# Optimization experiments

Hardware: AMD Instinct MI355X
Metric: run time of the kernel (lower is better)

The kernel has to match this reference:

```python
import jax, jax.numpy as jnp
import numpy as np

# Dropout layers are treated as identity (eval mode); note the original Adaptive
# module references self.dropout without defining it, so train mode would error anyway.

def setup_inputs() -> dict:
    key = jax.random.key(0)
    ks = jax.random.split(key, 13)
    B, T, H, E2, VOC, K = 128, 64, 512, 1024, 10000, 49
    s = lambda *sh: 1.0 / np.sqrt(sh[-1])
    return {
        "x":       jax.random.normal(ks[0], (B, T, E2), jnp.float32),
        "hiddens": jax.random.normal(ks[1], (B, T, H), jnp.float32),
        "cells":   jax.random.normal(ks[2], (B, T, H), jnp.float32),
        "V":       jax.random.normal(ks[3], (B, K, H), jnp.float32),
        # attention params
        "Wv": jax.random.normal(ks[4], (K, H), jnp.float32) * s(K, H),
        "Wg": jax.random.normal(ks[5], (K, H), jnp.float32) * s(K, H),
        "Ws": jax.random.normal(ks[6], (K, H), jnp.float32) * s(K, H),
        "wh": jax.random.normal(ks[7], (K,), jnp.float32) * s(K,),
        # sentinel params
        "Wx":  jax.random.normal(ks[8], (H, E2), jnp.float32) * s(H, E2),
        "Wsh": jax.random.normal(ks[9], (H, H), jnp.float32) * s(H, H),
        # output mlp
        "Wm": jax.random.normal(ks[10], (VOC, H), jnp.float32) * s(VOC, H),
        "bm": jnp.zeros((VOC,), jnp.float32),
    }


def reference(x, hiddens, cells, V, Wv, Wg, Ws, wh, Wx, Wsh, Wm, bm):
    B, T, H = hiddens.shape
    # h_{t-1}: zero init state prepended, last hidden dropped
    h0 = jnp.zeros((B, 1, H), hiddens.dtype)
    hiddens_t_1 = jnp.concatenate([h0, hiddens[:, :-1, :]], axis=1) if T > 1 else h0

    # Sentinel gate: sent_t = sigmoid(x Wx^T + h_{t-1} Wh^T) * tanh(cells)
    gate = jnp.einsum('bte,he->bth', x, Wx) + jnp.einsum('btj,hj->bth', hiddens_t_1, Wsh)
    sent = jax.nn.sigmoid(gate) * jnp.tanh(cells)            # [B,T,H]

    # Additive attention over K=49 spatial features
    cv = jnp.einsum('bkh,nh->bkn', V, Wv)                    # [B,K,49]
    cg = jnp.einsum('bth,nh->btn', hiddens, Wg)              # [B,T,49]
    content = jnp.tanh(cv[:, None, :, :] + cg[:, :, None, :])  # [B,T,K,49]
    z = jnp.einsum('btkn,n->btk', content, wh)               # [B,T,K]
    alpha = jax.nn.softmax(z, axis=-1)                       # [B,T,K]
    c = jnp.einsum('btk,bkh->bth', alpha, V)                 # [B,T,H]

    # Sentinel-extended softmax -> beta
    cs = jnp.einsum('bth,nh->btn', sent, Ws) + cg            # [B,T,49]
    z_ext = jnp.einsum('btn,n->bt', jnp.tanh(cs), wh)[..., None]  # [B,T,1]
    extend = jnp.concatenate([z, z_ext], axis=-1)            # [B,T,K+1]
    alpha_hat = jax.nn.softmax(extend, axis=-1)
    beta = alpha_hat[:, :, -1:]                              # [B,T,1]

    c_hat = beta * sent + (1.0 - beta) * c                   # [B,T,H]
    output = jnp.einsum('bth,vh->btv', c_hat + hiddens, Wm) + bm  # [B,T,vocab]
    return output, alpha, beta
```

## Files before the change

### kernel.cpp

```cpp
#include <hip/hip_runtime.h>
#include <hip/hip_bf16.h>
#include <math.h>

typedef __bf16 bf16;
typedef __bf16 bf16x4 __attribute__((ext_vector_type(4)));
typedef __bf16 bf16x8 __attribute__((ext_vector_type(8)));
typedef float f32x4 __attribute__((ext_vector_type(4)));

#define BB  128
#define TT  64
#define BTT 8192
#define HH  512
#define EE  1024
#define KA  49
#define NV  10000

__device__ __forceinline__ float ftanh(float x) {
    float cx = fminf(fmaxf(x, -15.f), 15.f);
    float e = __expf(2.f * cx);
    return (e - 1.f) * __builtin_amdgcn_rcpf(e + 1.f);
}
__device__ __forceinline__ float fsigmoid(float x) {
    return __builtin_amdgcn_rcpf(1.f + __expf(-x));
}

__device__ __forceinline__ void cvt4(const float* __restrict__ s, bf16* __restrict__ d) {
    f32x4 v = *(const f32x4*)s;
    bf16x4 o = { (bf16)v[0], (bf16)v[1], (bf16)v[2], (bf16)v[3] };
    *(bf16x4*)d = o;
}
__device__ __forceinline__ void cvt4nt(const float* __restrict__ s, bf16* __restrict__ d) {
    f32x4 v = __builtin_nontemporal_load((const f32x4*)s);
    bf16x4 o = { (bf16)v[0], (bf16)v[1], (bf16)v[2], (bf16)v[3] };
    *(bf16x4*)d = o;
}

__global__ __launch_bounds__(256)
void prep_kernel(const float* __restrict__ x, const float* __restrict__ hid,
                 const float* __restrict__ V, const float* __restrict__ Wv,
                 const float* __restrict__ Wg, const float* __restrict__ Ws,
                 const float* __restrict__ Wx, const float* __restrict__ Wsh,
                 bf16* __restrict__ xb, bf16* __restrict__ hb, bf16* __restrict__ hpb,
                 bf16* __restrict__ Vb, bf16* __restrict__ Wvb, bf16* __restrict__ Wgb,
                 bf16* __restrict__ Wsb, bf16* __restrict__ Wxb, bf16* __restrict__ Wshb)
{
    const long NX = (long)BTT * EE;
    const long NH = (long)BTT * HH;
    const long NVV = (long)BB * KA * HH;
    const long NWX = (long)HH * EE;
    const long NWSH = (long)HH * HH;
    const long NW = (long)KA * HH;
    const long total4 = (NX + NH + NH + NVV + NWX + NWSH + 3 * NW) >> 2;

    long t0 = (long)blockIdx.x * 256 + threadIdx.x;
    long st = (long)gridDim.x * 256;
    for (long i4 = t0; i4 < total4; i4 += st) {
        long i = i4 << 2;
        if (i < NX) { cvt4nt(x + i, xb + i); continue; }
        i -= NX;
        if (i < NH) { cvt4(hid + i, hb + i); continue; }
        i -= NH;
        if (i < NH) {
            long t = (i >> 9) & (TT - 1);
            if (t == 0) { bf16x4 z = {}; *(bf16x4*)(hpb + i) = z; }
            else cvt4(hid + i - HH, hpb + i);
            continue;
        }
        i -= NH;
        if (i < NVV) { cvt4nt(V + i, Vb + i); continue; }
        i -= NVV;
        if (i < NWX) { cvt4nt(Wx + i, Wxb + i); continue; }
        i -= NWX;
        if (i < NWSH) { cvt4nt(Wsh + i, Wshb + i); continue; }
        i -= NWSH;
        if (i < NW) { cvt4nt(Wv + i, Wvb + i); continue; }
        i -= NW;
        if (i < NW) { cvt4nt(Wg + i, Wgb + i); continue; }
        i -= NW;
        cvt4nt(Ws + i, Wsb + i);
    }
}

template<int EPI>
__device__ __forceinline__ void gemm128_core(
    bf16* smem,
    const bf16* __restrict__ A1, const bf16* __restrict__ B1, int K1,
    const bf16* __restrict__ A2, const bf16* __restrict__ B2, int K2,
    int N, const float* __restrict__ eaux, void* __restrict__ outv, int ldo,
    int bm0, int bn0)
{
    const int tid = threadIdx.x;
    const int lane = tid & 63;
    const int wid = tid >> 6;
    const int wm = (wid >> 1) * 64;
    const int wn = (wid & 1) * 64;
    const int rA = lane & 15;
    const int ks = lane >> 4;
    const int swzB = (ks ^ ((rA >> 1) & 3)) * 16;

    const int c0 = tid, c1 = tid + 256;
    const int row0 = c0 >> 2, row1 = c1 >> 2;
    const int gc0 = ((c0 & 3) ^ ((row0 >> 1) & 3)) * 8;
    const int gc1 = ((c1 & 3) ^ ((row1 >> 1) & 3)) * 8;
    const int br0 = (bn0 + row0 < N) ? bn0 + row0 : N - 1;
    const int br1 = (bn0 + row1 < N) ? bn0 + row1 : N - 1;

    const int NT1 = K1 >> 5;
    const int NT2 = K2 >> 5;
    const int NT = NT1 + NT2;

    auto stage = [&](int t) {
        const bf16 *Ap, *Bp; int K, k0;
        if (t < NT1) { Ap = A1; Bp = B1; K = K1; k0 = t << 5; }
        else         { Ap = A2; Bp = B2; K = K2; k0 = (t - NT1) << 5; }
        char* base = (char*)smem + (t & 3) * 16384;
        __builtin_amdgcn_global_load_lds(
            (const __attribute__((address_space(1))) unsigned int*)(Ap + (size_t)(bm0 + row0) * K + k0 + gc0),
            (__attribute__((address_space(3))) unsigned int*)(base + c0 * 16), 16, 0, 0);
        __builtin_amdgcn_global_load_lds(
            (const __attribute__((address_space(1))) unsigned int*)(Ap + (size_t)(bm0 + row1) * K + k0 + gc1),
            (__attribute__((address_space(3))) unsigned int*)(base + c1 * 16), 16, 0, 0);
        __builtin_amdgcn_global_load_lds(
            (const __attribute__((address_space(1))) unsigned int*)(Bp + (size_t)br0 * K + k0 + gc0),
            (__attribute__((address_space(3))) unsigned int*)(base + 8192 + c0 * 16), 16, 0, 0);
        __builtin_amdgcn_global_load_lds(
            (const __attribute__((address_space(1))) unsigned int*)(Bp + (size_t)br1 * K + k0 + gc1),
            (__attribute__((address_space(3))) unsigned int*)(base + 8192 + c1 * 16), 16, 0, 0);
    };

    f32x4 acc[4][4] = {};

    stage(0); stage(1); stage(2);
    asm volatile("s_waitcnt vmcnt(8)" ::: "memory");
    __builtin_amdgcn_s_barrier();

    for (int t = 0; t < NT; ++t) {
        const char* sA = (const char*)smem + (t & 3) * 16384;
        const char* sB = sA + 8192;

        bf16x8 af[4], bfr[4];
        #pragma unroll
        for (int mi = 0; mi < 4; ++mi)
            af[mi] = *(const bf16x8*)(sA + (wm + mi * 16 + rA) * 64 + swzB);
        #pragma unroll
        for (int ni = 0; ni < 4; ++ni)
            bfr[ni] = *(const bf16x8*)(sB + (wn + ni * 16 + rA) * 64 + swzB);

        if (t + 3 < NT) {
            stage(t + 3);
            asm volatile("s_waitcnt vmcnt(8)" ::: "memory");
        } else if (t + 2 < NT) {
            asm volatile("s_waitcnt vmcnt(4)" ::: "memory");
        } else {
            asm volatile("s_waitcnt vmcnt(0)" ::: "memory");
        }
        __builtin_amdgcn_s_barrier();

        __builtin_amdgcn_s_setprio(1);
        #pragma unroll
        for (int mi = 0; mi < 4; ++mi) {
            #pragma unroll
            for (int ni = 0; ni < 4; ++ni)
                acc[mi][ni] = __builtin_amdgcn_mfma_f32_16x16x32_bf16(af[mi], bfr[ni], acc[mi][ni], 0, 0, 0);
        }
        __builtin_amdgcn_s_setprio(0);
        __builtin_amdgcn_s_barrier();
    }

    #pragma unroll
    for (int mi = 0; mi < 4; ++mi) {
        #pragma unroll
        for (int ni = 0; ni < 4; ++ni) {
            const int col = bn0 + wn + ni * 16 + rA;
            if (col < N) {
                #pragma unroll
                for (int r = 0; r < 4; ++r) {
                    const int rowg = bm0 + wm + mi * 16 + ks * 4 + r;
                    float v = acc[mi][ni][r];
                    if (EPI == 0) {
                        ((bf16*)outv)[(size_t)rowg * ldo + col] =
                            (bf16)(fsigmoid(v) * ftanh(eaux[(size_t)rowg * ldo + col]));
                    } else {
                        ((float*)outv)[(size_t)rowg * ldo + col] = v;
                    }
                }
            }
        }
    }
}

__global__ __launch_bounds__(256, 2)
void gate_mid128(const bf16* __restrict__ xb, const bf16* __restrict__ Wxb,
                 const bf16* __restrict__ hpb, const bf16* __restrict__ Wshb,
                 const float* __restrict__ cel, bf16* __restrict__ sentb,
                 const bf16* __restrict__ Vb, const bf16* __restrict__ Wvb,
                 const bf16* __restrict__ hb, const bf16* __restrict__ Wgb,
                 float* __restrict__ cv, float* __restrict__ cg,
                 const float* __restrict__ Wm, bf16* __restrict__ Wmb)
{
    __shared__ bf16 smem[4 * 8192];
    const int bid = blockIdx.x;
    if (bid >= 369) {
        const long n4 = ((long)NV * HH) >> 2;
        for (long i4 = (long)(bid - 369) * 256 + threadIdx.x; i4 < n4; i4 += 143L * 256)
            cvt4nt(Wm + (i4 << 2), Wmb + (i4 << 2));
        return;
    }
    if (bid < 256) {
        const int bm0 = (bid >> 2) * 128;
        const int bn0 = (bid & 3) * 128;
        gemm128_core<0>(smem, xb, Wxb, EE, hpb, Wshb, HH, HH, cel, (void*)sentb, HH, bm0, bn0);
    } else if (bid < 305) {
        gemm128_core<2>(smem, Vb, Wvb, HH, nullptr, nullptr, 0, KA, nullptr, (void*)cv, KA,
                        (bid - 256) * 128, 0);
    } else {
        gemm128_core<2>(smem, hb, Wgb, HH, nullptr, nullptr, 0, KA, nullptr, (void*)cg, KA,
                        (bid - 305) * 128, 0);
    }
}

__global__ __launch_bounds__(256, 2)
void cs128(const bf16* __restrict__ sentb, const bf16* __restrict__ Wsb,
           const bf16* __restrict__ hb, const bf16* __restrict__ Wgb,
           float* __restrict__ cs)
{
    __shared__ bf16 smem[4 * 8192];
    gemm128_core<2>(smem, sentb, Wsb, HH, hb, Wgb, HH, KA, nullptr, (void*)cs, KA,
                    blockIdx.x * 128, 0);
}

__global__ __launch_bounds__(512, 4)
void gemm256x128_bias(const bf16* __restrict__ A, const bf16* __restrict__ B,
                      const float* __restrict__ bias, float* __restrict__ out)
{
    const int K = HH;
    const int N = NV;
    const int NT = K / 32;
    const int ntn = 79;

    __shared__ bf16 smem[3 * 12288];

    const int bid = blockIdx.x;
    const int wg = (bid & 7) * 316 + (bid >> 3);
    const int bm0 = (wg / ntn) * 256;
    const int bn0 = (wg % ntn) * 128;

    const int tid = threadIdx.x;
    const int lane = tid & 63;
    const int wid = tid >> 6;
    const int wr = (wid >> 1) * 64;
    const int wc = (wid & 1) * 64;
    const int rA = lane & 15;
    const int ks = lane >> 4;
    const int swz = (ks ^ ((rA >> 1) & 3)) * 16;

    const int arow0 = tid >> 2;
    const int arow1 = arow0 + 128;
    const int gcA0 = ((tid & 3) ^ ((arow0 >> 1) & 3)) * 8;
    const int gcA1 = ((tid & 3) ^ ((arow1 >> 1) & 3)) * 8;
    const int brow = tid >> 2;
    const int gcB  = ((tid & 3) ^ ((brow >> 1) & 3)) * 8;
    const int browc = (bn0 + brow < N) ? bn0 + brow : N - 1;

    const bf16* Ap0 = A + (size_t)(bm0 + arow0) * K + gcA0;
    const bf16* Ap1 = A + (size_t)(bm0 + arow1) * K + gcA1;
    const bf16* Bp  = B + (size_t)browc * K + gcB;

    auto stage = [&](int t, int slot) {
        char* base = (char*)smem + slot * 24576;
        const int k0 = t << 5;
        __builtin_amdgcn_global_load_lds(
            (const __attribute__((address_space(1))) unsigned int*)(Ap0 + k0),
            (__attribute__((address_space(3))) unsigned int*)(base + tid * 16), 16, 0, 0);
        __builtin_amdgcn_global_load_lds(
            (const __attribute__((address_space(1))) unsigned int*)(Ap1 + k0),
            (__attribute__((address_space(3))) unsigned int*)(base + (tid + 512) * 16), 16, 0, 0);
        __builtin_amdgcn_global_load_lds(
            (const __attribute__((address_space(1))) unsigned int*)(Bp + k0),
            (__attribute__((address_space(3))) unsigned int*)(base + 16384 + tid * 16), 16, 0, 0);
    };

    f32x4 acc[4][4] = {};

    stage(0, 0); stage(1, 1);
    asm volatile("s_waitcnt vmcnt(3)" ::: "memory");
    __builtin_amdgcn_s_barrier();

    int slR = 0, slS = 2;
    for (int t = 0; t < NT; ++t) {
        const char* sA = (const char*)smem + slR * 24576;
        const char* sB = sA + 16384;

        bf16x8 af[4], bfr[4];
        #pragma unroll
        for (int mi = 0; mi < 4; ++mi)
            af[mi] = *(const bf16x8*)(sA + (wr + mi * 16 + rA) * 64 + swz);
        #pragma unroll
        for (int ni = 0; ni < 4; ++ni)
            bfr[ni] = *(const bf16x8*)(sB + (wc + ni * 16 + rA) * 64 + swz);

        if (t + 2 < NT) {
            stage(t + 2, slS);
            asm volatile("s_waitcnt vmcnt(3)" ::: "memory");
        } else {
            asm volatile("s_waitcnt vmcnt(0)" ::: "memory");
        }
        __builtin_amdgcn_s_barrier();

        __builtin_amdgcn_s_setprio(1);
        #pragma unroll
        for (int mi = 0; mi < 4; ++mi) {
            #pragma unroll
            for (int ni = 0; ni < 4; ++ni)
                acc[mi][ni] = __builtin_amdgcn_mfma_f32_16x16x32_bf16(af[mi], bfr[ni], acc[mi][ni], 0, 0, 0);
        }
        __builtin_amdgcn_s_setprio(0);
        __builtin_amdgcn_s_barrier();

        slR = (slR == 2) ? 0 : slR + 1;
        slS = (slS == 2) ? 0 : slS + 1;
    }

    float bv[4];
    #pragma unroll
    for (int ni = 0; ni < 4; ++ni) {
        const int col = bn0 + wc + ni * 16 + rA;
        bv[ni] = (col < N) ? bias[col] : 0.f;
    }
    #pragma unroll
    for (int mi = 0; mi < 4; ++mi) {
        #pragma unroll
        for (int ni = 0; ni < 4; ++ni) {
            const int col = bn0 + wc + ni * 16 + rA;
            if (col < N) {
                #pragma unroll
                for (int r = 0; r < 4; ++r) {
                    const int rowg = bm0 + wr + mi * 16 + ks * 4 + r;
                    __builtin_nontemporal_store(acc[mi][ni][r] + bv[ni],
                                                &out[(size_t)rowg * N + col]);
                }
            }
        }
    }
}

__global__ __launch_bounds__(256)
void softz_kernel(const float* __restrict__ cv, const float* __restrict__ cg,
                  const float* __restrict__ cs, const float* __restrict__ wh,
                  float* __restrict__ alpha, float* __restrict__ beta)
{
    __shared__ float cvL[KA * KA];
    __shared__ float whL[64];
    __shared__ float cgL[4 * KA];

    const int tid = threadIdx.x;
    const int w = tid >> 6, lane = tid & 63;
    const int bt0 = blockIdx.x * 4;
    const int b = bt0 >> 6;
    const int bt = bt0 + w;

    const float* cvb = cv + (size_t)b * KA * KA;
    for (int i = tid; i < KA * KA; i += 256) cvL[i] = cvb[i];
    if (tid < KA) whL[tid] = wh[tid];
    if (lane < KA) cgL[w * KA + lane] = cg[(size_t)bt * KA + lane];
    float csv = (lane < KA) ? cs[(size_t)bt * KA + lane] : 0.f;
    __syncthreads();

    float z = -INFINITY;
    if (lane < KA) {
        const float* cvk = cvL + lane * KA;
        const float* cgr = cgL + w * KA;
        float acc = 0.f;
        #pragma unroll 7
        for (int n = 0; n < KA; ++n)
            acc += ftanh(cvk[n] + cgr[n]) * whL[n];
        z = acc;
    }
    float u = (lane < KA) ? ftanh(csv) * whL[lane] : 0.f;

    float m1 = z;
    #pragma unroll
    for (int o = 32; o; o >>= 1) m1 = fmaxf(m1, __shfl_xor(m1, o, 64));
    float e = (lane < KA) ? __expf(z - m1) : 0.f;
    float s1 = e, ze = u;
    #pragma unroll
    for (int o = 32; o; o >>= 1) { s1 += __shfl_xor(s1, o, 64); ze += __shfl_xor(ze, o, 64); }

    if (lane < KA) alpha[(size_t)bt * KA + lane] = e / s1;
    if (lane == 0) {
        float M2 = fmaxf(m1, ze);
        float denom = s1 * __expf(m1 - M2) + __expf(ze - M2);
        beta[bt] = __expf(ze - M2) / denom;
    }
}

__global__ __launch_bounds__(256)
void cch_kernel(const float* __restrict__ alpha, const float* __restrict__ beta,
                const bf16* __restrict__ Vb, const bf16* __restrict__ sentb,
                const float* __restrict__ hid, bf16* __restrict__ chb)
{
    __shared__ float aL[TT * KA];
    __shared__ float bL[TT];

    const int b = blockIdx.x >> 3;
    const int hc = blockIdx.x & 7;
    const int tid = threadIdx.x;
    const int w = tid >> 6, lane = tid & 63;
    const int h = hc * 64 + lane;

    const float* ab = alpha + (size_t)b * TT * KA;
    for (int i = tid; i < TT * KA; i += 256) aL[i] = ab[i];
    if (tid < TT) bL[tid] = beta[b * TT + tid];

    float vreg[KA];
    #pragma unroll
    for (int k = 0; k < KA; ++k) vreg[k] = (float)Vb[((size_t)b * KA + k) * HH + h];
    __syncthreads();

    #pragma unroll 1
    for (int tt = 0; tt < 16; ++tt) {
        const int t = w * 16 + tt;
        const int bt = b * TT + t;
        const float* ar = aL + t * KA;
        float c = 0.f;
        #pragma unroll
        for (int k = 0; k < KA; ++k) c += ar[k] * vreg[k];
        const float be = bL[t];
        const size_t idx = (size_t)bt * HH + h;
        float ch = be * (float)sentb[idx] + (1.f - be) * c
                 + __builtin_nontemporal_load(hid + idx);
        chb[idx] = (bf16)ch;
    }
}

extern "C" void kernel_launch(void* const* d_in, const int* in_sizes, int n_in,
                              void* d_out, int out_size, void* d_ws, size_t ws_size,
                              hipStream_t stream)
{
    const float* x   = (const float*)d_in[0];
    const float* hid = (const float*)d_in[1];
    const float* cel = (const float*)d_in[2];
    const float* V   = (const float*)d_in[3];
    const float* Wv  = (const float*)d_in[4];
    const float* Wg  = (const float*)d_in[5];
    const float* Ws  = (const float*)d_in[6];
    const float* wh  = (const float*)d_in[7];
    const float* Wx  = (const float*)d_in[8];
    const float* Wsh = (const float*)d_in[9];
    const float* Wm  = (const float*)d_in[10];
    const float* bm  = (const float*)d_in[11];

    float* out_o   = (float*)d_out;
    float* alpha_o = out_o + (size_t)BTT * NV;
    float* beta_o  = alpha_o + (size_t)BTT * KA;

    char* p = (char*)d_ws;
    bf16* sentb = (bf16*)p; p += (size_t)BTT * HH * 2;
    bf16* chb   = (bf16*)p; p += (size_t)BTT * HH * 2;
    bf16* xb    = (bf16*)p; p += (size_t)BTT * EE * 2;
    bf16* hb    = (bf16*)p; p += (size_t)BTT * HH * 2;
    bf16* hpb   = (bf16*)p; p += (size_t)BTT * HH * 2;
    bf16* Vb    = (bf16*)p; p += (size_t)BB * KA * HH * 2;
    bf16* Wxb   = (bf16*)p; p += (size_t)HH * EE * 2;
    bf16* Wshb  = (bf16*)p; p += (size_t)HH * HH * 2;
    bf16* Wmb   = (bf16*)p; p += (size_t)NV * HH * 2;
    bf16* Wvb   = (bf16*)p; p += (size_t)KA * HH * 2;
    bf16* Wgb   = (bf16*)p; p += (size_t)KA * HH * 2;
    bf16* Wsb   = (bf16*)p; p += (size_t)KA * HH * 2;
    float* cv   = (float*)p; p += (size_t)BB * KA * KA * 4;
    float* cg   = (float*)p; p += (size_t)BTT * KA * 4;
    float* cs   = (float*)p; p += (size_t)BTT * KA * 4;

    prep_kernel<<<2048, 256, 0, stream>>>(x, hid, V, Wv, Wg, Ws, Wx, Wsh,
                                          xb, hb, hpb, Vb, Wvb, Wgb, Wsb, Wxb, Wshb);

    gate_mid128<<<512, 256, 0, stream>>>(xb, Wxb, hpb, Wshb, cel, sentb,
                                         Vb, Wvb, hb, Wgb, cv, cg, Wm, Wmb);

    cs128<<<64, 256, 0, stream>>>(sentb, Wsb, hb, Wgb, cs);

    softz_kernel<<<BTT / 4, 256, 0, stream>>>(cv, cg, cs, wh, alpha_o, beta_o);
    cch_kernel<<<BB * 8, 256, 0, stream>>>(alpha_o, beta_o, Vb, sentb, hid, chb);

    gemm256x128_bias<<<32 * 79, 512, 0, stream>>>(chb, Wmb, bm, out_o);
}
```

Measured before the change: 240.0 us.

## Drop shifted-hidden buffer via row-offset pointers and stage output GEMM stores through LDS

The separate bf16 copy of the time-shifted hidden states is removed. The gate GEMM now reads rows of the plain hidden buffer offset by one, and a small zero buffer stands in for the first timestep, which saves one full conversion write and read. Per-row operand base pointers are precomputed outside the staging lambda. The final vocab GEMM epilogue now transposes accumulators through swizzled LDS so each lane can issue 16-byte nontemporal vector stores instead of scalar stores. This assumes the LDS is free after the main loop and that N is a multiple of 4 for the column guard.

```diff
diff --git a/kernel.cpp b/kernel.cpp
--- a/kernel.cpp
+++ b/kernel.cpp
@@ -40,17 +40,23 @@
                  const float* __restrict__ V, const float* __restrict__ Wv,
                  const float* __restrict__ Wg, const float* __restrict__ Ws,
                  const float* __restrict__ Wx, const float* __restrict__ Wsh,
-                 bf16* __restrict__ xb, bf16* __restrict__ hb, bf16* __restrict__ hpb,
+                 bf16* __restrict__ xb, bf16* __restrict__ hb,
                  bf16* __restrict__ Vb, bf16* __restrict__ Wvb, bf16* __restrict__ Wgb,
-                 bf16* __restrict__ Wsb, bf16* __restrict__ Wxb, bf16* __restrict__ Wshb)
-{
+                 bf16* __restrict__ Wsb, bf16* __restrict__ Wxb, bf16* __restrict__ Wshb,
+                 bf16* __restrict__ zbuf)
+{
+    if (blockIdx.x == 0 && threadIdx.x < 128) {
+        bf16x8 z = {};
+        *(bf16x8*)(zbuf + threadIdx.x * 8) = z;
+    }
+
     const long NX = (long)BTT * EE;
     const long NH = (long)BTT * HH;
     const long NVV = (long)BB * KA * HH;
     const long NWX = (long)HH * EE;
     const long NWSH = (long)HH * HH;
     const long NW = (long)KA * HH;
-    const long total4 = (NX + NH + NH + NVV + NWX + NWSH + 3 * NW) >> 2;
+    const long total4 = (NX + NH + NVV + NWX + NWSH + 3 * NW) >> 2;
 
     long t0 = (long)blockIdx.x * 256 + threadIdx.x;
     long st = (long)gridDim.x * 256;
@@ -59,13 +65,6 @@
         if (i < NX) { cvt4nt(x + i, xb + i); continue; }
         i -= NX;
         if (i < NH) { cvt4(hid + i, hb + i); continue; }
-        i -= NH;
-        if (i < NH) {
-            long t = (i >> 9) & (TT - 1);
-            if (t == 0) { bf16x4 z = {}; *(bf16x4*)(hpb + i) = z; }
-            else cvt4(hid + i - HH, hpb + i);
-            continue;
-        }
         i -= NH;
         if (i < NVV) { cvt4nt(V + i, Vb + i); continue; }
         i -= NVV;
@@ -81,13 +80,13 @@
     }
 }
 
-template<int EPI>
+template<int EPI, bool SHIFT>
 __device__ __forceinline__ void gemm128_core(
     bf16* smem,
     const bf16* __restrict__ A1, const bf16* __restrict__ B1, int K1,
     const bf16* __restrict__ A2, const bf16* __restrict__ B2, int K2,
     int N, const float* __restrict__ eaux, void* __restrict__ outv, int ldo,
-    int bm0, int bn0)
+    int bm0, int bn0, const bf16* __restrict__ zbuf)
 {
     const int tid = threadIdx.x;
     const int lane = tid & 63;
@@ -109,22 +108,41 @@
     const int NT2 = K2 >> 5;
     const int NT = NT1 + NT2;
 
+    const bf16* A1r0 = A1 + (size_t)(bm0 + row0) * K1 + gc0;
+    const bf16* A1r1 = A1 + (size_t)(bm0 + row1) * K1 + gc1;
+    const bf16* B1r0 = B1 + (size_t)br0 * K1 + gc0;
+    const bf16* B1r1 = B1 + (size_t)br1 * K1 + gc1;
+    const bf16 *A2r0 = nullptr, *A2r1 = nullptr, *B2r0 = nullptr, *B2r1 = nullptr;
+    if (K2 > 0) {
+        if (SHIFT) {
+            A2r0 = (((bm0 + row0) & 63) == 0) ? zbuf + gc0
+                                              : A2 + (size_t)(bm0 + row0 - 1) * K2 + gc0;
+            A2r1 = (((bm0 + row1) & 63) == 0) ? zbuf + gc1
+                                              : A2 + (size_t)(bm0 + row1 - 1) * K2 + gc1;
+        } else {
+            A2r0 = A2 + (size_t)(bm0 + row0) * K2 + gc0;
+            A2r1 = A2 + (size_t)(bm0 + row1) * K2 + gc1;
+        }
+        B2r0 = B2 + (size_t)br0 * K2 + gc0;
+        B2r1 = B2 + (size_t)br1 * K2 + gc1;
+    }
+
     auto stage = [&](int t) {
-        const bf16 *Ap, *Bp; int K, k0;
-        if (t < NT1) { Ap = A1; Bp = B1; K = K1; k0 = t << 5; }
-        else         { Ap = A2; Bp = B2; K = K2; k0 = (t - NT1) << 5; }
+        const bf16 *a0, *a1, *b0, *b1; int k0;
+        if (t < NT1) { k0 = t << 5;          a0 = A1r0; a1 = A1r1; b0 = B1r0; b1 = B1r1; }
+        else         { k0 = (t - NT1) << 5;  a0 = A2r0; a1 = A2r1; b0 = B2r0; b1 = B2r1; }
         char* base = (char*)smem + (t & 3) * 16384;
         __builtin_amdgcn_global_load_lds(
-            (const __attribute__((address_space(1))) unsigned int*)(Ap + (size_t)(bm0 + row0) * K + k0 + gc0),
+            (const __attribute__((address_space(1))) unsigned int*)(a0 + k0),
             (__attribute__((address_space(3))) unsigned int*)(base + c0 * 16), 16, 0, 0);
         __builtin_amdgcn_global_load_lds(
-            (const __attribute__((address_space(1))) unsigned int*)(Ap + (size_t)(bm0 + row1) * K + k0 + gc1),
+            (const __attribute__((address_space(1))) unsigned int*)(a1 + k0),
             (__attribute__((address_space(3))) unsigned int*)(base + c1 * 16), 16, 0, 0);
         __builtin_amdgcn_global_load_lds(
-            (const __attribute__((address_space(1))) unsigned int*)(Bp + (size_t)br0 * K + k0 + gc0),
+            (const __attribute__((address_space(1))) unsigned int*)(b0 + k0),
             (__attribute__((address_space(3))) unsigned int*)(base + 8192 + c0 * 16), 16, 0, 0);
         __builtin_amdgcn_global_load_lds(
-            (const __attribute__((address_space(1))) unsigned int*)(Bp + (size_t)br1 * K + k0 + gc1),
+            (const __attribute__((address_space(1))) unsigned int*)(b1 + k0),
             (__attribute__((address_space(3))) unsigned int*)(base + 8192 + c1 * 16), 16, 0, 0);
     };
 
@@ -191,12 +209,13 @@
 
 __global__ __launch_bounds__(256, 2)
 void gate_mid128(const bf16* __restrict__ xb, const bf16* __restrict__ Wxb,
-                 const bf16* __restrict__ hpb, const bf16* __restrict__ Wshb,
+                 const bf16* __restrict__ Wshb,
                  const float* __restrict__ cel, bf16* __restrict__ sentb,
                  const bf16* __restrict__ Vb, const bf16* __restrict__ Wvb,
                  const bf16* __restrict__ hb, const bf16* __restrict__ Wgb,
                  float* __restrict__ cv, float* __restrict__ cg,
-                 const float* __restrict__ Wm, bf16* __restrict__ Wmb)
+                 const float* __restrict__ Wm, bf16* __restrict__ Wmb,
+                 const bf16* __restrict__ zbuf)
 {
     __shared__ bf16 smem[4 * 8192];
     const int bid = blockIdx.x;
@@ -209,13 +228,14 @@
     if (bid < 256) {
         const int bm0 = (bid >> 2) * 128;
         const int bn0 = (bid & 3) * 128;
-        gemm128_core<0>(smem, xb, Wxb, EE, hpb, Wshb, HH, HH, cel, (void*)sentb, HH, bm0, bn0);
+        gemm128_core<0, true>(smem, xb, Wxb, EE, hb, Wshb, HH, HH, cel, (void*)sentb, HH,
+                              bm0, bn0, zbuf);
     } else if (bid < 305) {
-        gemm128_core<2>(smem, Vb, Wvb, HH, nullptr, nullptr, 0, KA, nullptr, (void*)cv, KA,
-                        (bid - 256) * 128, 0);
+        gemm128_core<2, false>(smem, Vb, Wvb, HH, nullptr, nullptr, 0, KA, nullptr,
+                               (void*)cv, KA, (bid - 256) * 128, 0, nullptr);
     } else {
-        gemm128_core<2>(smem, hb, Wgb, HH, nullptr, nullptr, 0, KA, nullptr, (void*)cg, KA,
-                        (bid - 305) * 128, 0);
+        gemm128_core<2, false>(smem, hb, Wgb, HH, nullptr, nullptr, 0, KA, nullptr,
+                               (void*)cg, KA, (bid - 305) * 128, 0, nullptr);
     }
 }
 
@@ -225,8 +245,8 @@
            float* __restrict__ cs)
 {
     __shared__ bf16 smem[4 * 8192];
-    gemm128_core<2>(smem, sentb, Wsb, HH, hb, Wgb, HH, KA, nullptr, (void*)cs, KA,
-                    blockIdx.x * 128, 0);
+    gemm128_core<2, false>(smem, sentb, Wsb, HH, hb, Wgb, HH, KA, nullptr, (void*)cs, KA,
+                           blockIdx.x * 128, 0, nullptr);
 }
 
 __global__ __launch_bounds__(512, 4)
@@ -327,19 +347,33 @@
         const int col = bn0 + wc + ni * 16 + rA;
         bv[ni] = (col < N) ? bias[col] : 0.f;
     }
+    float* lt = (float*)smem + wid * 2048;
     #pragma unroll
-    for (int mi = 0; mi < 4; ++mi) {
-        #pragma unroll
-        for (int ni = 0; ni < 4; ++ni) {
-            const int col = bn0 + wc + ni * 16 + rA;
-            if (col < N) {
+    for (int half = 0; half < 2; ++half) {
+        #pragma unroll
+        for (int mi2 = 0; mi2 < 2; ++mi2) {
+            const int mi = half * 2 + mi2;
+            #pragma unroll
+            for (int ni = 0; ni < 4; ++ni) {
                 #pragma unroll
                 for (int r = 0; r < 4; ++r) {
-                    const int rowg = bm0 + wr + mi * 16 + ks * 4 + r;
-                    __builtin_nontemporal_store(acc[mi][ni][r] + bv[ni],
-                                                &out[(size_t)rowg * N + col]);
+                    const int row = mi2 * 16 + ks * 4 + r;
+                    const int col = ni * 16 + rA;
+                    const int s = ((((row >> 2) & 3) ^ (row & 3)) << 4);
+                    lt[row * 64 + (col ^ s)] = acc[mi][ni][r] + bv[ni];
                 }
             }
+        }
+        #pragma unroll
+        for (int i = 0; i < 8; ++i) {
+            const int row = i * 4 + ks;
+            const int c0 = rA * 4;
+            const int s = ((((row >> 2) & 3) ^ (row & 3)) << 4);
+            f32x4 v = *(const f32x4*)&lt[row * 64 + (c0 ^ s)];
+            const int rowg = bm0 + wr + half * 32 + row;
+            const int colg = bn0 + wc + c0;
+            if (colg < N)
+                __builtin_nontemporal_store(v, (f32x4*)&out[(size_t)rowg * N + colg]);
         }
     }
 }
@@ -459,7 +493,6 @@
     bf16* chb   = (bf16*)p; p += (size_t)BTT * HH * 2;
     bf16* xb    = (bf16*)p; p += (size_t)BTT * EE * 2;
     bf16* hb    = (bf16*)p; p += (size_t)BTT * HH * 2;
-    bf16* hpb   = (bf16*)p; p += (size_t)BTT * HH * 2;
     bf16* Vb    = (bf16*)p; p += (size_t)BB * KA * HH * 2;
     bf16* Wxb   = (bf16*)p; p += (size_t)HH * EE * 2;
     bf16* Wshb  = (bf16*)p; p += (size_t)HH * HH * 2;
@@ -467,15 +500,16 @@
     bf16* Wvb   = (bf16*)p; p += (size_t)KA * HH * 2;
     bf16* Wgb   = (bf16*)p; p += (size_t)KA * HH * 2;
     bf16* Wsb   = (bf16*)p; p += (size_t)KA * HH * 2;
+    bf16* zbuf  = (bf16*)p; p += 1024 * 2;
     float* cv   = (float*)p; p += (size_t)BB * KA * KA * 4;
     float* cg   = (float*)p; p += (size_t)BTT * KA * 4;
     float* cs   = (float*)p; p += (size_t)BTT * KA * 4;
 
     prep_kernel<<<2048, 256, 0, stream>>>(x, hid, V, Wv, Wg, Ws, Wx, Wsh,
-                                          xb, hb, hpb, Vb, Wvb, Wgb, Wsb, Wxb, Wshb);
-
-    gate_mid128<<<512, 256, 0, stream>>>(xb, Wxb, hpb, Wshb, cel, sentb,
-                                         Vb, Wvb, hb, Wgb, cv, cg, Wm, Wmb);
+                                          xb, hb, Vb, Wvb, Wgb, Wsb, Wxb, Wshb, zbuf);
+
+    gate_mid128<<<512, 256, 0, stream>>>(xb, Wxb, Wshb, cel, sentb,
+                                         Vb, Wvb, hb, Wgb, cv, cg, Wm, Wmb, zbuf);
 
     cs128<<<64, 256, 0, stream>>>(sentb, Wsb, hb, Wgb, cs);
 
```

After: 226.8 us. 5.5% less time.
